# Kernel tuning notes

Measured on AMD Instinct MI355X. Metric: run time of the kernel, lower is better.

Reference implementation:

```python
import jax, jax.numpy as jnp
import numpy as np

B, S, D, H = 4, 2048, 1024, 16
DK = D // H


def setup_inputs() -> dict:
    key = jax.random.key(0)
    ks = jax.random.split(key, 5)
    init_std = np.sqrt(2.0 / (D + D))  # trunc bound proxy; plain randn clamped below
    trunc = 3 * init_std

    def w(k):
        return jnp.clip(jax.random.normal(k, (D, D), dtype=jnp.float32), -trunc, trunc)

    x = jax.random.normal(ks[0], (B, S, D), dtype=jnp.float32)
    return {
        "x": x,
        "W_Q": w(ks[1]),
        "W_K": w(ks[2]),
        "W_V": w(ks[3]),
        "W_O": w(ks[4]),
        "is_causal": 1,
    }


def reference(x, W_Q, W_K, W_V, W_O, is_causal):
    b, s, d = x.shape
    # Linear: y = W @ x with W:[out,in], x:[..., in]
    def proj(W, t):
        y = jnp.einsum("oi,bsi->bso", W, t)
        # [b, s, h*dk] -> [b, h, s, dk]
        return y.reshape(b, s, H, DK).transpose(0, 2, 1, 3)

    q = proj(W_Q, x)
    k = proj(W_K, x)
    v = proj(W_V, x)

    scores = jnp.einsum("bhqd,bhkd->bhqk", q, k) * (DK ** -0.5)
    if is_causal:
        causal = jnp.tril(jnp.ones((s, s), dtype=bool))
        scores = jnp.where(causal, scores, -jnp.inf)
    attn = jax.nn.softmax(scores, axis=-1)
    out = jnp.einsum("bhqk,bhkd->bhqd", attn, v)
    out = out.transpose(0, 2, 1, 3).reshape(b, s, H * DK)
    return jnp.einsum("oi,bsi->bso", W_O, out)
```

## Files before the change

### kernel.cpp

```cpp
#include <hip/hip_runtime.h>
#include <stdint.h>

#define NB 4
#define NS 2048
#define ND 1024
#define NH 16
#define NDK 64
#define L2E 1.44269504088896340736f
#define AS1 __attribute__((address_space(1)))
#define AS3 __attribute__((address_space(3)))

typedef __attribute__((ext_vector_type(8)))  short     s16x8;
typedef __attribute__((ext_vector_type(4)))  float     f32x4;
typedef __attribute__((ext_vector_type(16))) float     f32x16;
typedef __attribute__((ext_vector_type(4)))  unsigned  u32x4;

__device__ __forceinline__ unsigned short f2bf(float f) {
    union { float f; unsigned u; } v; v.f = f;
    unsigned r = v.u + 0x7FFFu + ((v.u >> 16) & 1u);
    return (unsigned short)(r >> 16);
}
__device__ __forceinline__ unsigned cvt_pk_bf16(float lo, float hi) {
    unsigned r;
    asm("v_cvt_pk_bf16_f32 %0, %1, %2" : "=v"(r) : "v"(lo), "v"(hi));
    return r;
}
__device__ __forceinline__ void pl32swap(unsigned &a, unsigned &b) {
    asm volatile("v_permlane32_swap_b32 %0, %1" : "+v"(a), "+v"(b));
}
__device__ __forceinline__ float exp2_hw(float x) {
    float r; asm("v_exp_f32 %0, %1" : "=v"(r) : "v"(x)); return r;
}
__device__ __forceinline__ f32x16 fz16() {
    f32x16 z;
#pragma unroll
    for (int r = 0; r < 16; ++r) z[r] = 0.f;
    return z;
}
__device__ __forceinline__ f32x16 mfma32(const s16x8& a, const s16x8& b, const f32x16& c) {
    return __builtin_amdgcn_mfma_f32_32x32x16_bf16(a, b, c, 0, 0, 0);
}

__global__ void convert_all(const void* __restrict__ x,  const void* __restrict__ wq,
                            const void* __restrict__ wk, const void* __restrict__ wv,
                            unsigned short* __restrict__ XB, unsigned short* __restrict__ WQKV,
                            int* __restrict__ flag) {
    __shared__ int sfl;
    int tid = threadIdx.x;
    if (tid < 64) {
        int cnt = 0;
        const unsigned* xw = (const unsigned*)x;
        for (int i = tid; i < 1024; i += 64) {
            unsigned lo = xw[i] & 0xFFFFu;
            unsigned e  = (lo >> 7) & 0xFFu;
            cnt += (e >= 100u && e <= 140u) ? 1 : 0;
        }
        for (int d = 1; d < 64; d <<= 1) cnt += __shfl_xor(cnt, d);
        if (tid == 0) {
            sfl = (cnt > 512) ? 1 : 0;
            if (blockIdx.x == 0) flag[0] = sfl;
        }
    }
    __syncthreads();
    int fl = sfl;

    const int A  = (NB * NS * ND) / 8;
    const int WC = (ND * ND) / 8;
    int i = blockIdx.x * blockDim.x + tid;
    int stride = gridDim.x * blockDim.x;
    int total = A + 3 * WC;
    for (; i < total; i += stride) {
        const void* src; unsigned short* dst; long o8;
        if (i < A) { src = x; dst = XB; o8 = i; }
        else {
            int k = i - A, which = k >> 17, o = k & (WC - 1);
            src = which == 0 ? wq : (which == 1 ? wk : wv);
            dst = WQKV + (long)which * (ND * ND);
            o8 = o;
        }
        u32x4 v;
        if (fl) {
            v = *(const u32x4*)((const unsigned short*)src + o8 * 8);
        } else {
            const float* p = (const float*)src + o8 * 8;
            f32x4 a = *(const f32x4*)p;
            f32x4 b = *(const f32x4*)(p + 4);
            v[0] = cvt_pk_bf16(a[0], a[1]);
            v[1] = cvt_pk_bf16(a[2], a[3]);
            v[2] = cvt_pk_bf16(b[0], b[1]);
            v[3] = cvt_pk_bf16(b[2], b[3]);
        }
        *(u32x4*)(dst + o8 * 8) = v;
    }
}

__global__ void convert_bf16(const void* __restrict__ src, unsigned short* __restrict__ dst,
                             int n8, const int* __restrict__ flagp) {
    int i = blockIdx.x * blockDim.x + threadIdx.x;
    int stride = gridDim.x * blockDim.x;
    int fl = *flagp;
    for (; i < n8; i += stride) {
        u32x4 v;
        if (fl) {
            v = *(const u32x4*)((const unsigned short*)src + (long)i * 8);
        } else {
            const float* p = (const float*)src + (long)i * 8;
            f32x4 a = *(const f32x4*)p;
            f32x4 b = *(const f32x4*)(p + 4);
            v[0] = cvt_pk_bf16(a[0], a[1]);
            v[1] = cvt_pk_bf16(a[2], a[3]);
            v[2] = cvt_pk_bf16(b[0], b[1]);
            v[3] = cvt_pk_bf16(b[2], b[3]);
        }
        *(u32x4*)(dst + (long)i * 8) = v;
    }
}

__device__ __forceinline__ void stage_glds64(const unsigned short* __restrict__ src, int ld,
                                             long r0, int k0, unsigned short* lds, int tid) {
#pragma unroll
    for (int h = 0; h < 4; ++h) {
        int c = h * 256 + tid;
        int row = c >> 3;
        int scol = (c & 7) ^ (row & 7);
        const unsigned short* gp = src + (r0 + row) * ld + k0 + scol * 8;
        unsigned short* lp = lds + (c & ~63) * 8;
        __builtin_amdgcn_global_load_lds(
            (const AS1 unsigned short*)gp, (AS3 unsigned short*)lp, 16, 0, 0);
    }
}

template<int OUT_MODE, int NXB>
__global__ __launch_bounds__(256, 2)
void gemm3(const unsigned short* __restrict__ A, const unsigned short* __restrict__ W,
           void* __restrict__ dst, const int* __restrict__ flagp, float scale)
{
    __shared__ unsigned short As[128 * 64];
    __shared__ unsigned short Bs[128 * 64];
    const long TOKc = (long)NB * NS * ND;
    int tid  = threadIdx.x;
    int w    = tid >> 6, lane = tid & 63;
    int wr   = w >> 1,   wc   = w & 1;
    int nwg = (int)(gridDim.x * gridDim.y);
    int bid = (int)(blockIdx.y * gridDim.x + blockIdx.x);
    int nb  = (bid & 7) * (nwg >> 3) + (bid >> 3);
    int n0  = (nb % NXB) * 128;
    long m0 = (long)(nb / NXB) * 128;
    int fl  = *flagp;

    f32x4 zero4 = {0.f, 0.f, 0.f, 0.f};
    f32x4 acc[4][4];
#pragma unroll
    for (int i = 0; i < 4; ++i)
#pragma unroll
        for (int j = 0; j < 4; ++j) acc[i][j] = zero4;

    int lr = lane & 15, lg = lane >> 4;

    for (int k0 = 0; k0 < 1024; k0 += 64) {
        __syncthreads();
        stage_glds64(A, 1024, m0, k0, As, tid);
        stage_glds64(W, 1024, n0, k0, Bs, tid);
        __syncthreads();
#pragma unroll
        for (int kk = 0; kk < 2; ++kk) {
            s16x8 af[4], bf[4];
#pragma unroll
            for (int i = 0; i < 4; ++i) {
                int row = wr * 64 + i * 16 + lr;
                int u = (kk * 4 + lg) ^ (lr & 7);
                af[i] = *(const s16x8*)(As + row * 64 + u * 8);
            }
#pragma unroll
            for (int j = 0; j < 4; ++j) {
                int row = wc * 64 + j * 16 + lr;
                int u = (kk * 4 + lg) ^ (lr & 7);
                bf[j] = *(const s16x8*)(Bs + row * 64 + u * 8);
            }
#pragma unroll
            for (int i = 0; i < 4; ++i)
#pragma unroll
                for (int j = 0; j < 4; ++j)
                    acc[i][j] = __builtin_amdgcn_mfma_f32_16x16x32_bf16(af[i], bf[j], acc[i][j], 0, 0, 0);
        }
    }

    int rbase = (lane >> 4) * 4;
#pragma unroll
    for (int i = 0; i < 4; ++i)
#pragma unroll
        for (int j = 0; j < 4; ++j)
#pragma unroll
            for (int r = 0; r < 4; ++r) {
                long m = m0 + wr * 64 + i * 16 + rbase + r;
                int  n = n0 + wc * 64 + j * 16 + lr;
                float v = acc[i][j][r];
                if (OUT_MODE == 3) {
                    long b = m >> 11, s = m & 2047;
                    int hh = (n >> 6) & 15, dk = n & 63;
                    float sc = (n < 1024) ? scale : 1.0f;
                    long off = (n >= 1024) ? TOKc : 0;
                    ((unsigned short*)dst)[off + (((b * NH + hh) * NS) + s) * NDK + dk] = f2bf(v * sc);
                } else if (OUT_MODE == 1) {
                    int hh = (int)(m >> 6), dk = (int)(m & 63);
                    long b = n >> 11, s = n & 2047;
                    ((unsigned short*)dst)[(((b * NH + hh) * NDK) + dk) * NS + s] = f2bf(v * scale);
                } else {
                    if (fl) ((unsigned short*)dst)[m * 1024 + n] = f2bf(v * scale);
                    else    ((float*)dst)[m * 1024 + n] = v * scale;
                }
            }
}

__device__ __forceinline__ void stage_tile64(const char* __restrict__ srcbase, int rowstride,
                                             unsigned short* lds, int tid) {
#pragma unroll
    for (int h = 0; h < 4; ++h) {
        int c = h * 128 + tid;
        int L = c * 16;
        int row = L >> 7;
        int sr  = (L & 127) ^ ((row & 7) << 4);
        const char* gp = srcbase + row * rowstride + sr;
        unsigned short* lp = lds + (c & ~63) * 8;
        __builtin_amdgcn_global_load_lds((const AS1 unsigned short*)gp,
                                         (AS3 unsigned short*)lp, 16, 0, 0);
    }
}

__device__ __forceinline__ void sm64s(f32x16& st0, f32x16& st1, float& l,
                                      bool mask, int kv0, int qb, int l31, int hi,
                                      s16x8* pf)
{
    if (mask) {
        int q = qb + l31;
#pragma unroll
        for (int r = 0; r < 16; ++r) {
            int crow = (r & 3) + 8 * (r >> 2) + 4 * hi;
            if (kv0 + crow > q)      st0[r] = -1e30f;
            if (kv0 + 32 + crow > q) st1[r] = -1e30f;
        }
    }
#pragma unroll
    for (int r = 0; r < 16; ++r) {
        st0[r] = exp2_hw(st0[r]);
        st1[r] = exp2_hw(st1[r]);
    }
    float s8[8];
#pragma unroll
    for (int r = 0; r < 8; ++r) s8[r] = (st0[r] + st0[r + 8]) + (st1[r] + st1[r + 8]);
    float s4[4];
#pragma unroll
    for (int r = 0; r < 4; ++r) s4[r] = s8[r] + s8[r + 4];
    l += (s4[0] + s4[1]) + (s4[2] + s4[3]);

#pragma unroll
    for (int half = 0; half < 2; ++half) {
        const f32x16& st = half ? st1 : st0;
        unsigned b0 = cvt_pk_bf16(st[0],  st[1]);
        unsigned b1 = cvt_pk_bf16(st[2],  st[3]);
        unsigned b2 = cvt_pk_bf16(st[4],  st[5]);
        unsigned b3 = cvt_pk_bf16(st[6],  st[7]);
        unsigned b4 = cvt_pk_bf16(st[8],  st[9]);
        unsigned b5 = cvt_pk_bf16(st[10], st[11]);
        unsigned b6 = cvt_pk_bf16(st[12], st[13]);
        unsigned b7 = cvt_pk_bf16(st[14], st[15]);
        pl32swap(b0, b2);  pl32swap(b1, b3);
        pl32swap(b4, b6);  pl32swap(b5, b7);
        union { unsigned u[4]; s16x8 v; } p0, p1;
        p0.u[0] = b0; p0.u[1] = b1; p0.u[2] = b2; p0.u[3] = b3;
        p1.u[0] = b4; p1.u[1] = b5; p1.u[2] = b6; p1.u[3] = b7;
        pf[half * 2]     = p0.v;
        pf[half * 2 + 1] = p1.v;
    }
}

__device__ __forceinline__ void attn_epi(unsigned short* epb, const f32x16& o0, const f32x16& o1,
                                         float lrow, int l31, int hi, int lane,
                                         unsigned short* __restrict__ Oo, int qb, int b, int hh)
{
    float lt = lrow + __shfl_xor(lrow, 32);
    float inv = 1.0f / lt;
#pragma unroll
    for (int j = 0; j < 2; ++j) {
        const f32x16& o = j ? o1 : o0;
#pragma unroll
        for (int g = 0; g < 4; ++g) {
            int d0 = j * 32 + g * 8 + hi * 4;
            unsigned lo = cvt_pk_bf16(o[g * 4 + 0] * inv, o[g * 4 + 1] * inv);
            unsigned hw = cvt_pk_bf16(o[g * 4 + 2] * inv, o[g * 4 + 3] * inv);
            unsigned short* p = epb + l31 * 72 + d0;
            *(unsigned*)(p)     = lo;
            *(unsigned*)(p + 2) = hw;
        }
    }
    asm volatile("s_waitcnt lgkmcnt(0)" ::: "memory");
    __builtin_amdgcn_sched_barrier(0);
#pragma unroll
    for (int rr = 0; rr < 4; ++rr) {
        int q2 = rr * 8 + (lane >> 3);
        int d2 = (lane & 7) * 8;
        u32x4 vv = *(const u32x4*)(epb + q2 * 72 + d2);
        *(u32x4*)(Oo + (((long)b * NS + qb + q2) * ND) + hh * NDK + d2) = vv;
    }
}

__global__ __launch_bounds__(128)
void attn_fwd12(const unsigned short* __restrict__ Q,
                const unsigned short* __restrict__ Kt,
                const unsigned short* __restrict__ Vt,
                unsigned short* __restrict__ Oo,
                const int* __restrict__ causalp)
{
    __shared__ char lds[2][16384];
    int tid = threadIdx.x, w = tid >> 6, lane = tid & 63;
    int l31 = lane & 31, hi = lane >> 5;
    int bh = blockIdx.x;
    int j  = 31 - (int)blockIdx.y;
    int t  = 2 * j + w, qb = t * 32;
    int causal = *causalp;
    int nst   = causal ? (j + 1) : (NS / 64);
    int sdiag = causal ? (t >> 1) : 0x7FFFFFFF;

    const unsigned short* Qh = Q  + bh * (NS * NDK);
    const char* Khb = (const char*)(Kt + (long)bh * NS * NDK);
    const char* Vhb = (const char*)(Vt + (long)bh * NDK * NS);

    s16x8 qf[4];
#pragma unroll
    for (int kd = 0; kd < 4; ++kd)
        qf[kd] = *(const s16x8*)(Qh + (qb + l31) * NDK + kd * 16 + hi * 8);

    int koff[4];
#pragma unroll
    for (int kd = 0; kd < 4; ++kd)
        koff[kd] = l31 * 128 + ((kd * 32 + hi * 16) ^ ((l31 & 7) << 4));

    const f32x16 Z16 = fz16();
    f32x16 o0 = fz16(), o1 = fz16();
    float l = 0.f;

    stage_tile64(Khb, 128, (unsigned short*)&lds[0][0], tid);
    stage_tile64(Vhb, NS * 2, (unsigned short*)&lds[0][8192], tid);
    __syncthreads();

    int cur = 0;
    for (int s = 0; s < nst; ++s) {
        if (s + 1 < nst) {
            int kv1 = (s + 1) * 64;
            stage_tile64(Khb + (long)kv1 * 128, 128, (unsigned short*)&lds[cur ^ 1][0], tid);
            stage_tile64(Vhb + kv1 * 2, NS * 2, (unsigned short*)&lds[cur ^ 1][8192], tid);
        }
        {
            const char* kb = &lds[cur][0];
            const char* vb = &lds[cur][8192];
            f32x16 st0, st1;
            __builtin_amdgcn_s_setprio(1);
            {
                s16x8 k0 = *(const s16x8*)(kb + koff[0]);
                s16x8 k1 = *(const s16x8*)(kb + 4096 + koff[0]);
                st0 = mfma32(k0, qf[0], Z16);
                st1 = mfma32(k1, qf[0], Z16);
            }
#pragma unroll
            for (int kd = 1; kd < 4; ++kd) {
                s16x8 k0 = *(const s16x8*)(kb + koff[kd]);
                s16x8 k1 = *(const s16x8*)(kb + 4096 + koff[kd]);
                st0 = mfma32(k0, qf[kd], st0);
                st1 = mfma32(k1, qf[kd], st1);
            }
            __builtin_amdgcn_s_setprio(0);
            s16x8 pf[4];
            sm64s(st0, st1, l, s == sdiag, s * 64, qb, l31, hi, pf);
            __builtin_amdgcn_s_setprio(1);
#pragma unroll
            for (int ks = 0; ks < 4; ++ks) {
                s16x8 va = *(const s16x8*)(vb + koff[ks]);
                s16x8 wb = *(const s16x8*)(vb + 4096 + koff[ks]);
                o0 = mfma32(va, pf[ks], o0);
                o1 = mfma32(wb, pf[ks], o1);
            }
            __builtin_amdgcn_s_setprio(0);
        }
        __syncthreads();
        cur ^= 1;
    }

    unsigned short* ep = (unsigned short*)&lds[0][0] + w * (32 * 72);
    attn_epi(ep, o0, o1, l, l31, hi, lane, Oo, qb, bh >> 4, bh & 15);
}

extern "C" void kernel_launch(void* const* d_in, const int* in_sizes, int n_in,
                              void* d_out, int out_size, void* d_ws, size_t ws_size,
                              hipStream_t stream) {
    const void* x  = d_in[0];
    const void* Wq = d_in[1];
    const void* Wk = d_in[2];
    const void* Wv = d_in[3];
    const void* Wo = d_in[4];
    const int* causal = (const int*)d_in[5];

    const long TOK  = (long)NB * NS * ND;
    const long WTOK = (long)ND * ND;
    size_t need = 256 + 4UL * TOK * 2;
    if (ws_size < need) return;

    char* ws = (char*)d_ws;
    int* flag = (int*)ws;
    unsigned short* Qb = (unsigned short*)(ws + 256);
    unsigned short* Kb = Qb + TOK;
    unsigned short* Vb = Kb + TOK;
    unsigned short* XB = Vb + TOK;
    unsigned short* Ab = XB;
    unsigned short* WOB = Qb;
    unsigned short* WQKV = (unsigned short*)((char*)d_out + (size_t)out_size * 2 - 3UL * WTOK * 2);

    convert_all<<<2048, 256, 0, stream>>>(x, Wq, Wk, Wv, XB, WQKV, flag);

    dim3 blk(256);
    gemm3<3, 16><<<dim3(16, 64), blk, 0, stream>>>(XB, WQKV, Qb, flag, 0.125f * L2E);
    gemm3<1, 64><<<dim3(64, 8), blk, 0, stream>>>(WQKV + 2 * WTOK, XB, Vb, flag, 1.0f);
    attn_fwd12<<<dim3(64, 32), 128, 0, stream>>>(Qb, Kb, Vb, Ab, causal);
    convert_bf16<<<512, 256, 0, stream>>>(Wo, WOB, (int)(WTOK / 8), flag);
    gemm3<2, 8><<<dim3(8, 64), blk, 0, stream>>>(Ab, WOB, d_out, flag, 1.0f);
}
```

Measured before the change: 166.1 us.

## Fuse V projection into QKV GEMM and widen attention blocks to four waves

The separate V-projection GEMM is folded into one QKV GEMM over 3072 output columns, and its epilogue writes V transposed directly. The attention kernel now runs four waves per block sharing each staged K/V tile, which halves the number of blocks and the total tile loads. The softmax row sum is computed by an extra MFMA against a ones vector instead of scalar adds and a cross-lane shuffle. This saves one launch and some global staging traffic, at the cost of extra MFMA work and per-wave imbalance: waves past the causal diagonal skip compute but still wait at every block barrier.

Result: no change. 168.9 us (+1.7%).

```diff
diff --git a/kernel.cpp b/kernel.cpp
--- a/kernel.cpp
+++ b/kernel.cpp
@@ -195,16 +195,16 @@
                 long m = m0 + wr * 64 + i * 16 + rbase + r;
                 int  n = n0 + wc * 64 + j * 16 + lr;
                 float v = acc[i][j][r];
-                if (OUT_MODE == 3) {
+                if (OUT_MODE == 4) {
                     long b = m >> 11, s = m & 2047;
                     int hh = (n >> 6) & 15, dk = n & 63;
-                    float sc = (n < 1024) ? scale : 1.0f;
-                    long off = (n >= 1024) ? TOKc : 0;
-                    ((unsigned short*)dst)[off + (((b * NH + hh) * NS) + s) * NDK + dk] = f2bf(v * sc);
-                } else if (OUT_MODE == 1) {
-                    int hh = (int)(m >> 6), dk = (int)(m & 63);
-                    long b = n >> 11, s = n & 2047;
-                    ((unsigned short*)dst)[(((b * NH + hh) * NDK) + dk) * NS + s] = f2bf(v * scale);
+                    if (n < 2048) {
+                        float sc = (n < 1024) ? scale : 1.0f;
+                        long off = (n >= 1024) ? TOKc : 0;
+                        ((unsigned short*)dst)[off + (((b * NH + hh) * NS) + s) * NDK + dk] = f2bf(v * sc);
+                    } else {
+                        ((unsigned short*)dst)[2 * TOKc + (((b * NH + hh) * NDK) + dk) * NS + s] = f2bf(v);
+                    }
                 } else {
                     if (fl) ((unsigned short*)dst)[m * 1024 + n] = f2bf(v * scale);
                     else    ((float*)dst)[m * 1024 + n] = v * scale;
@@ -215,8 +215,8 @@
 __device__ __forceinline__ void stage_tile64(const char* __restrict__ srcbase, int rowstride,
                                              unsigned short* lds, int tid) {
 #pragma unroll
-    for (int h = 0; h < 4; ++h) {
-        int c = h * 128 + tid;
+    for (int h = 0; h < 2; ++h) {
+        int c = h * 256 + tid;
         int L = c * 16;
         int row = L >> 7;
         int sr  = (L & 127) ^ ((row & 7) << 4);
@@ -227,7 +227,7 @@
     }
 }
 
-__device__ __forceinline__ void sm64s(f32x16& st0, f32x16& st1, float& l,
+__device__ __forceinline__ void sm64s(f32x16& st0, f32x16& st1,
                                       bool mask, int kv0, int qb, int l31, int hi,
                                       s16x8* pf)
 {
@@ -245,14 +245,6 @@
         st0[r] = exp2_hw(st0[r]);
         st1[r] = exp2_hw(st1[r]);
     }
-    float s8[8];
-#pragma unroll
-    for (int r = 0; r < 8; ++r) s8[r] = (st0[r] + st0[r + 8]) + (st1[r] + st1[r + 8]);
-    float s4[4];
-#pragma unroll
-    for (int r = 0; r < 4; ++r) s4[r] = s8[r] + s8[r + 4];
-    l += (s4[0] + s4[1]) + (s4[2] + s4[3]);
-
 #pragma unroll
     for (int half = 0; half < 2; ++half) {
         const f32x16& st = half ? st1 : st0;
@@ -275,11 +267,10 @@
 }
 
 __device__ __forceinline__ void attn_epi(unsigned short* epb, const f32x16& o0, const f32x16& o1,
-                                         float lrow, int l31, int hi, int lane,
+                                         float lsum, int l31, int hi, int lane,
                                          unsigned short* __restrict__ Oo, int qb, int b, int hh)
 {
-    float lt = lrow + __shfl_xor(lrow, 32);
-    float inv = 1.0f / lt;
+    float inv = 1.0f / lsum;
 #pragma unroll
     for (int j = 0; j < 2; ++j) {
         const f32x16& o = j ? o1 : o0;
@@ -304,8 +295,8 @@
     }
 }
 
-__global__ __launch_bounds__(128)
-void attn_fwd12(const unsigned short* __restrict__ Q,
+__global__ __launch_bounds__(256, 3)
+void attn_fwd14(const unsigned short* __restrict__ Q,
                 const unsigned short* __restrict__ Kt,
                 const unsigned short* __restrict__ Vt,
                 unsigned short* __restrict__ Oo,
@@ -315,10 +306,10 @@
     int tid = threadIdx.x, w = tid >> 6, lane = tid & 63;
     int l31 = lane & 31, hi = lane >> 5;
     int bh = blockIdx.x;
-    int j  = 31 - (int)blockIdx.y;
-    int t  = 2 * j + w, qb = t * 32;
+    int j  = 15 - (int)blockIdx.y;
+    int t  = 4 * j + w, qb = t * 32;
     int causal = *causalp;
-    int nst   = causal ? (j + 1) : (NS / 64);
+    int nst   = causal ? (2 * j + 2) : (NS / 64);
     int sdiag = causal ? (t >> 1) : 0x7FFFFFFF;
 
     const unsigned short* Qh = Q  + bh * (NS * NDK);
@@ -330,14 +321,17 @@
     for (int kd = 0; kd < 4; ++kd)
         qf[kd] = *(const s16x8*)(Qh + (qb + l31) * NDK + kd * 16 + hi * 8);
 
+    s16x8 onesv;
+#pragma unroll
+    for (int i = 0; i < 8; ++i) onesv[i] = (short)0x3F80;
+
     int koff[4];
 #pragma unroll
     for (int kd = 0; kd < 4; ++kd)
         koff[kd] = l31 * 128 + ((kd * 32 + hi * 16) ^ ((l31 & 7) << 4));
 
     const f32x16 Z16 = fz16();
-    f32x16 o0 = fz16(), o1 = fz16();
-    float l = 0.f;
+    f32x16 o0 = fz16(), o1 = fz16(), o2 = fz16();
 
     stage_tile64(Khb, 128, (unsigned short*)&lds[0][0], tid);
     stage_tile64(Vhb, NS * 2, (unsigned short*)&lds[0][8192], tid);
@@ -350,7 +344,7 @@
             stage_tile64(Khb + (long)kv1 * 128, 128, (unsigned short*)&lds[cur ^ 1][0], tid);
             stage_tile64(Vhb + kv1 * 2, NS * 2, (unsigned short*)&lds[cur ^ 1][8192], tid);
         }
-        {
+        if (s <= sdiag) {
             const char* kb = &lds[cur][0];
             const char* vb = &lds[cur][8192];
             f32x16 st0, st1;
@@ -370,7 +364,7 @@
             }
             __builtin_amdgcn_s_setprio(0);
             s16x8 pf[4];
-            sm64s(st0, st1, l, s == sdiag, s * 64, qb, l31, hi, pf);
+            sm64s(st0, st1, s == sdiag, s * 64, qb, l31, hi, pf);
             __builtin_amdgcn_s_setprio(1);
 #pragma unroll
             for (int ks = 0; ks < 4; ++ks) {
@@ -378,6 +372,7 @@
                 s16x8 wb = *(const s16x8*)(vb + 4096 + koff[ks]);
                 o0 = mfma32(va, pf[ks], o0);
                 o1 = mfma32(wb, pf[ks], o1);
+                o2 = mfma32(onesv, pf[ks], o2);
             }
             __builtin_amdgcn_s_setprio(0);
         }
@@ -386,7 +381,7 @@
     }
 
     unsigned short* ep = (unsigned short*)&lds[0][0] + w * (32 * 72);
-    attn_epi(ep, o0, o1, l, l31, hi, lane, Oo, qb, bh >> 4, bh & 15);
+    attn_epi(ep, o0, o1, o2[0], l31, hi, lane, Oo, qb, bh >> 4, bh & 15);
 }
 
 extern "C" void kernel_launch(void* const* d_in, const int* in_sizes, int n_in,
@@ -417,9 +412,8 @@
     convert_all<<<2048, 256, 0, stream>>>(x, Wq, Wk, Wv, XB, WQKV, flag);
 
     dim3 blk(256);
-    gemm3<3, 16><<<dim3(16, 64), blk, 0, stream>>>(XB, WQKV, Qb, flag, 0.125f * L2E);
-    gemm3<1, 64><<<dim3(64, 8), blk, 0, stream>>>(WQKV + 2 * WTOK, XB, Vb, flag, 1.0f);
-    attn_fwd12<<<dim3(64, 32), 128, 0, stream>>>(Qb, Kb, Vb, Ab, causal);
+    gemm3<4, 24><<<dim3(24, 64), blk, 0, stream>>>(XB, WQKV, Qb, flag, 0.125f * L2E);
+    attn_fwd14<<<dim3(64, 16), blk, 0, stream>>>(Qb, Kb, Vb, Ab, causal);
     convert_bf16<<<512, 256, 0, stream>>>(Wo, WOB, (int)(WTOK / 8), flag);
     gemm3<2, 8><<<dim3(8, 64), blk, 0, stream>>>(Ab, WOB, d_out, flag, 1.0f);
 }
```
